# Performance work log

Measured on AMD Instinct MI355X. Metric: run time of the kernel, lower is better.

The kernel has to match this reference:

```python
import jax, jax.numpy as jnp
import numpy as np

DIM = 2048
DT_RANK = 64
DIM_INNER = 2048
D_STATE = 32
B_SZ = 4
L = 2048


def setup_inputs() -> dict:
    key = jax.random.key(0)
    ks = jax.random.split(key, 6)
    x = jax.random.normal(ks[0], (B_SZ, L, DIM), dtype=jnp.float32)
    z = jax.random.normal(ks[1], (B_SZ, L, DIM_INNER), dtype=jnp.float32)
    # proj_bc: Linear(dim, dt_rank + 2*d_state, bias=False)
    W_bc = jax.random.normal(ks[2], (DT_RANK + 2 * D_STATE, DIM), dtype=jnp.float32) * (DIM ** -0.5)
    # dt_proj: maps dt_rank -> dim_inner (as intended in Mamba)
    W_dt = jax.random.normal(ks[3], (DIM_INNER, DT_RANK), dtype=jnp.float32) * (DT_RANK ** -0.5)
    b_dt = jax.random.normal(ks[4], (DIM_INNER,), dtype=jnp.float32) * 0.1
    # A = arange(1, d_state+1) repeated per channel; A_log = log(A)
    A_log = jnp.log(jnp.tile(jnp.arange(1, D_STATE + 1, dtype=jnp.float32), (DIM_INNER, 1)))
    D_param = jnp.ones((DIM_INNER,), dtype=jnp.float32)
    return {"x": x, "z": z, "W_bc": W_bc, "W_dt": W_dt, "b_dt": b_dt, "A_log": A_log, "D_param": D_param}


def _selective_scan(u, delta, A, Bm, Cm, D_param):
    # u, delta: [b, l, d]; Bm, Cm: [b, l, n]; A: [d, n]; D_param: [d]
    def step(h, inp):
        delta_t, B_t, C_t, u_t = inp  # [b,d], [b,n], [b,n], [b,d]
        dA = jnp.exp(delta_t[:, :, None] * A[None])          # [b, d, n]
        dBu = (delta_t * u_t)[:, :, None] * B_t[:, None, :]  # [b, d, n]
        h = dA * h + dBu
        y_t = jnp.einsum('bdn,bn->bd', h, C_t)
        return h, y_t

    b = u.shape[0]
    h0 = jnp.zeros((b, A.shape[0], A.shape[1]), dtype=u.dtype)
    xs = (jnp.moveaxis(delta, 1, 0), jnp.moveaxis(Bm, 1, 0),
          jnp.moveaxis(Cm, 1, 0), jnp.moveaxis(u, 1, 0))
    _, ys = jax.lax.scan(step, h0, xs)          # ys: [l, b, d]
    y = jnp.moveaxis(ys, 0, 1)                  # [b, l, d]
    return y + u * D_param[None, None, :]


def reference(x, z, W_bc, W_dt, b_dt, A_log, D_param):
    A = -jnp.exp(A_log)                                      # [d, n]
    deltaBC = jnp.einsum('bld,od->blo', x, W_bc)             # [b, l, r+2n]
    dt_r = deltaBC[..., :DT_RANK]
    Bm = deltaBC[..., DT_RANK:DT_RANK + D_STATE]             # [b, l, n]
    Cm = deltaBC[..., DT_RANK + D_STATE:]                    # [b, l, n]
    dt = jnp.einsum('blr,dr->bld', dt_r, W_dt)               # [b, l, d]
    delta = jax.nn.softplus(dt + b_dt[None, None, :])        # delta_softplus + delta_bias
    y = _selective_scan(x, delta, A, Bm, Cm, D_param)        # [b, l, d]
    return y
```

## Files before the change

### kernel.cpp

```cpp
#include <hip/hip_runtime.h>

#define L_SEQ 2048
#define NDIM 2048
#define DINNER 2048
#define NSTATE 32
#define BSZ 4
#define DTR 64
#define NROWS (BSZ * L_SEQ)
#define TCH 32

typedef short bf16x8 __attribute__((ext_vector_type(8)));
typedef float f32x4 __attribute__((ext_vector_type(4)));
typedef float f32x2 __attribute__((ext_vector_type(2)));
typedef unsigned int uint_t;

#if __has_builtin(__builtin_amdgcn_exp2f)
#define EXP2(v) __builtin_amdgcn_exp2f(v)
#else
#define EXP2(v) exp2f(v)
#endif
#define LOG2E 1.44269504f

__device__ __forceinline__ uint_t bf1(float a) {
  uint_t u = __float_as_uint(a);
  return (u + 0x7FFFu + ((u >> 16) & 1u)) >> 16;
}
__device__ __forceinline__ uint_t pkbf(float a, float b) {
  return bf1(a) | (bf1(b) << 16);
}

#define WBC_ELEMS (128 * NDIM)
#define WDT_ELEMS (DINNER * DTR)
__global__ __launch_bounds__(256) void k_conv(const float* __restrict__ Wbc,
                                              const float* __restrict__ Wdt,
                                              unsigned short* __restrict__ o) {
  const int i = blockIdx.x * 256 + threadIdx.x;
  if (i < WBC_ELEMS)
    o[i] = (unsigned short)bf1(Wbc[i]);
  else
    o[i] = (unsigned short)bf1(Wdt[i - WBC_ELEMS]);
}

__global__ __launch_bounds__(512) void k_dbc_mfma(const float* __restrict__ x,
                                                  const unsigned short* __restrict__ Wb,
                                                  float* __restrict__ dbc) {
  __shared__ unsigned short xl[32][72];
  __shared__ unsigned short wl[128][72];
  const int tid = threadIdx.x;
  const int wave = tid >> 6, lane = tid & 63;
  const int row0 = blockIdx.x * 32;
  const int wrow0 = (wave & 1) * 16;
  const int wcol0 = (wave >> 1) * 32;
  const int fr = lane & 15, fk = (lane >> 4) * 8;

  f32x4 acc[2];
#pragma unroll
  for (int i = 0; i < 2; ++i) acc[i] = (f32x4)(0.f);

  const int xr = tid >> 4, xk = (tid & 15) * 4;
  const int wc = tid & 127, wh = (tid >> 7) * 16;

  for (int kb = 0; kb < NDIM; kb += 64) {
    const float4 xa = *(const float4*)(x + (size_t)(row0 + xr) * NDIM + kb + xk);
    uint4 wv0 = *(const uint4*)(Wb + (size_t)wc * NDIM + kb + wh);
    uint4 wv1 = *(const uint4*)(Wb + (size_t)wc * NDIM + kb + wh + 8);
    __syncthreads();
    uint2 xp = {pkbf(xa.x, xa.y), pkbf(xa.z, xa.w)};
    *(uint2*)&xl[xr][xk] = xp;
    *(uint4*)&wl[wc][wh] = wv0;
    *(uint4*)&wl[wc][wh + 8] = wv1;
    __syncthreads();
#pragma unroll
    for (int ks = 0; ks < 2; ++ks) {
      const bf16x8 af = *(const bf16x8*)&xl[wrow0 + fr][ks * 32 + fk];
#pragma unroll
      for (int nt = 0; nt < 2; ++nt) {
        const bf16x8 bfv = *(const bf16x8*)&wl[wcol0 + nt * 16 + fr][ks * 32 + fk];
        acc[nt] = __builtin_amdgcn_mfma_f32_16x16x32_bf16(af, bfv, acc[nt], 0, 0, 0);
      }
    }
  }
#pragma unroll
  for (int nt = 0; nt < 2; ++nt)
#pragma unroll
    for (int reg = 0; reg < 4; ++reg)
      dbc[(size_t)(row0 + wrow0 + (lane >> 4) * 4 + reg) * 128 + wcol0 + nt * 16 + fr] =
          acc[nt][reg];
}

__global__ __launch_bounds__(256) void k_dt_mfma(const float* __restrict__ dbc,
                                                 const unsigned short* __restrict__ Wd,
                                                 const float* __restrict__ bdt,
                                                 float* __restrict__ dy) {
  __shared__ unsigned short al[32][72];
  const int tid = threadIdx.x;
  const int wave = tid >> 6, lane = tid & 63;
  const int row0 = blockIdx.y * 32;
  const int c0 = blockIdx.x * 256;
  const int wrow0 = (wave & 1) * 16;
  const int wc0 = c0 + (wave >> 1) * 128;
  const int fr = lane & 15, fk = (lane >> 4) * 8;

  {
    const int ar = tid >> 3, ak = (tid & 7) * 8;
    const float4 pa = *(const float4*)(dbc + (size_t)(row0 + ar) * 128 + ak);
    const float4 pb = *(const float4*)(dbc + (size_t)(row0 + ar) * 128 + ak + 4);
    uint4 ap = {pkbf(pa.x, pa.y), pkbf(pa.z, pa.w), pkbf(pb.x, pb.y), pkbf(pb.z, pb.w)};
    *(uint4*)&al[ar][ak] = ap;
  }
  __syncthreads();

  f32x4 acc[8];
#pragma unroll
  for (int i = 0; i < 8; ++i) acc[i] = (f32x4)(0.f);

#pragma unroll
  for (int ks = 0; ks < 2; ++ks) {
    const bf16x8 af = *(const bf16x8*)&al[wrow0 + fr][ks * 32 + fk];
#pragma unroll
    for (int nt = 0; nt < 8; ++nt) {
      const int col = wc0 + nt * 16 + fr;
      const bf16x8 bfv = *(const bf16x8*)(Wd + (size_t)col * 64 + ks * 32 + fk);
      acc[nt] = __builtin_amdgcn_mfma_f32_16x16x32_bf16(af, bfv, acc[nt], 0, 0, 0);
    }
  }

#pragma unroll
  for (int nt = 0; nt < 8; ++nt) {
    const int col = wc0 + nt * 16 + fr;
    const float bias = bdt[col];
#pragma unroll
    for (int reg = 0; reg < 4; ++reg) {
      const float v = acc[nt][reg] + bias;
      const float sp = (v > 20.f) ? v : __logf(1.f + __expf(v));
      dy[(size_t)(row0 + wrow0 + (lane >> 4) * 4 + reg) * DINNER + col] = sp;
    }
  }
}

__global__ __launch_bounds__(256) void k_dbc(const float* __restrict__ x,
                                             const float* __restrict__ Wbc,
                                             float* __restrict__ dbc) {
  __shared__ float xs[32][36];
  __shared__ float ws[32][132];
  const int tid = threadIdx.x;
  const int tx = tid & 31;
  const int ty = tid >> 5;
  const int row0 = blockIdx.x * 32;
  float acc[4][4];
#pragma unroll
  for (int i = 0; i < 4; ++i)
#pragma unroll
    for (int j = 0; j < 4; ++j) acc[i][j] = 0.f;
  for (int kb = 0; kb < NDIM; kb += 32) {
    {
      const int r = tid >> 3;
      const int k0 = (tid & 7) * 4;
      const float4 v = *(const float4*)(x + (size_t)(row0 + r) * NDIM + kb + k0);
      *(float4*)&xs[r][k0] = v;
    }
    {
      const int col = tid & 127;
      const int k0 = (tid >> 7) * 16;
#pragma unroll
      for (int j = 0; j < 4; ++j) {
        const float4 v = *(const float4*)(Wbc + (size_t)col * NDIM + kb + k0 + j * 4);
        ws[k0 + j * 4 + 0][col] = v.x;
        ws[k0 + j * 4 + 1][col] = v.y;
        ws[k0 + j * 4 + 2][col] = v.z;
        ws[k0 + j * 4 + 3][col] = v.w;
      }
    }
    __syncthreads();
#pragma unroll
    for (int k = 0; k < 32; k += 4) {
      float a_[4][4];
#pragma unroll
      for (int i = 0; i < 4; ++i) {
        const float4 av = *(const float4*)&xs[ty * 4 + i][k];
        a_[i][0] = av.x; a_[i][1] = av.y; a_[i][2] = av.z; a_[i][3] = av.w;
      }
#pragma unroll
      for (int kk = 0; kk < 4; ++kk) {
        const float4 bv = *(const float4*)&ws[k + kk][tx * 4];
        float b_[4] = {bv.x, bv.y, bv.z, bv.w};
#pragma unroll
        for (int i = 0; i < 4; ++i)
#pragma unroll
          for (int j = 0; j < 4; ++j)
            acc[i][j] = fmaf(a_[i][kk], b_[j], acc[i][j]);
      }
    }
    __syncthreads();
  }
#pragma unroll
  for (int i = 0; i < 4; ++i) {
    float4 o = {acc[i][0], acc[i][1], acc[i][2], acc[i][3]};
    *(float4*)(dbc + (size_t)(row0 + ty * 4 + i) * 128 + tx * 4) = o;
  }
}

__global__ __launch_bounds__(256) void k_dt(const float* __restrict__ dbc,
                                            const float* __restrict__ Wdt,
                                            const float* __restrict__ bdt,
                                            float* dy) {
  __shared__ float asn[16][68];
  __shared__ float wst[64][132];
  const int tid = threadIdx.x;
  const int tx = tid & 31;
  const int ty = tid >> 5;
  const int row0 = blockIdx.y * 16;
  const int col0 = blockIdx.x * 128;
  {
    const int r = tid >> 4;
    const int k0 = (tid & 15) * 4;
    const float4 v = *(const float4*)(dbc + (size_t)(row0 + r) * 128 + k0);
    *(float4*)&asn[r][k0] = v;
  }
  {
    const int col = tid & 127;
    const int k0 = (tid >> 7) * 32;
#pragma unroll
    for (int j = 0; j < 8; ++j) {
      const float4 v = *(const float4*)(Wdt + (size_t)(col0 + col) * 64 + k0 + j * 4);
      wst[k0 + j * 4 + 0][col] = v.x;
      wst[k0 + j * 4 + 1][col] = v.y;
      wst[k0 + j * 4 + 2][col] = v.z;
      wst[k0 + j * 4 + 3][col] = v.w;
    }
  }
  __syncthreads();
  float acc[2][4];
#pragma unroll
  for (int i = 0; i < 2; ++i)
#pragma unroll
    for (int j = 0; j < 4; ++j) acc[i][j] = 0.f;
#pragma unroll
  for (int k = 0; k < 64; k += 4) {
    float a_[2][4];
#pragma unroll
    for (int i = 0; i < 2; ++i) {
      const float4 av = *(const float4*)&asn[ty * 2 + i][k];
      a_[i][0] = av.x; a_[i][1] = av.y; a_[i][2] = av.z; a_[i][3] = av.w;
    }
#pragma unroll
    for (int kk = 0; kk < 4; ++kk) {
      const float4 bv = *(const float4*)&wst[k + kk][tx * 4];
      float b_[4] = {bv.x, bv.y, bv.z, bv.w};
#pragma unroll
      for (int i = 0; i < 2; ++i)
#pragma unroll
        for (int j = 0; j < 4; ++j)
          acc[i][j] = fmaf(a_[i][kk], b_[j], acc[i][j]);
    }
  }
  const int c = col0 + tx * 4;
  const float4 bb = *(const float4*)(bdt + c);
  const float bias[4] = {bb.x, bb.y, bb.z, bb.w};
#pragma unroll
  for (int i = 0; i < 2; ++i) {
    float o[4];
#pragma unroll
    for (int j = 0; j < 4; ++j) {
      const float v = acc[i][j] + bias[j];
      o[j] = (v > 20.f) ? v : __logf(1.f + __expf(v));
    }
    float4 ov = {o[0], o[1], o[2], o[3]};
    *(float4*)(dy + (size_t)(row0 + ty * 2 + i) * DINNER + c) = ov;
  }
}

template <int CTRL>
__device__ __forceinline__ float dpp_mov(float v) {
  return __int_as_float(
      __builtin_amdgcn_update_dpp(0, __float_as_int(v), CTRL, 0xF, 0xF, true));
}
__device__ __forceinline__ float red16(float p) {
  p += dpp_mov<0xB1>(p);
  p += dpp_mov<0x4E>(p);
  p += dpp_mov<0x141>(p);
  p += dpp_mov<0x140>(p);
  return p;
}

__global__ __launch_bounds__(256) void k_scanp(const float* __restrict__ x,
                                               const float* __restrict__ dbc,
                                               const float* __restrict__ Alog,
                                               const float* __restrict__ Dpar,
                                               float* __restrict__ dy) {
  __shared__ float sDU[2][16][68];
  __shared__ float sBCp[2][32][68];
  __shared__ float sY[2][32][17];

  const int tid = threadIdx.x;
  const int ln = tid & 15, ch = tid >> 4;
  const int dd = tid & 15, tl = tid >> 4;
  const int nb = tid & 31, tq = tid >> 5;
  const int dg = blockIdx.x & 127;
  const int b = blockIdx.x >> 7;
  const int d0 = dg * 16;
  const int NCHK = L_SEQ / TCH;

  f32x2 An2;
  An2.x = -__expf(Alog[(size_t)(d0 + ch) * NSTATE + ln]) * LOG2E;
  An2.y = -__expf(Alog[(size_t)(d0 + ch) * NSTATE + ln + 16]) * LOG2E;
  const float Dd = Dpar[d0 + dd];
  const size_t segbase = (size_t)b * L_SEQ;

  const int bccol = (nb & 15) * 4 + (nb >> 4) * 2;

  float u0, u1;
  {
    const size_t rX0 = (segbase + tl) * DINNER + d0 + dd;
    const size_t rX1 = (segbase + tl + 16) * DINNER + d0 + dd;
    const float dv0 = dy[rX0], uv0 = x[rX0];
    const float dv1 = dy[rX1], uv1 = x[rX1];
    *(float2*)&sDU[0][dd][(tl >> 1) * 4 + (tl & 1) * 2] = make_float2(dv0, dv0 * uv0);
    *(float2*)&sDU[0][(tl >> 1) + 8][0] = *(float2*)&sDU[0][(tl >> 1) + 8][0];
    *(float2*)&sDU[0][dd][((tl + 16) >> 1) * 4 + (tl & 1) * 2] =
        make_float2(dv1, dv1 * uv1);
    u0 = uv0;
    u1 = uv1;
#pragma unroll
    for (int k = 0; k < 4; ++k) {
      const int t = tq + k * 8;
      const size_t rB = (segbase + t) * 128 + 64 + nb;
      *(float2*)&sBCp[0][t][bccol] = make_float2(dbc[rB], dbc[rB + 32]);
    }
  }
  __syncthreads();

  f32x2 h = (f32x2)(0.f);
  for (int c = 0; c < NCHK; ++c) {
    const int cb = c & 1;
    float dn0 = 0.f, un0 = 0.f, dn1 = 0.f, un1 = 0.f;
    float2 bcx[4];
#pragma unroll
    for (int k = 0; k < 4; ++k) bcx[k] = make_float2(0.f, 0.f);
    if (c < NCHK - 1) {
      const size_t rX0 = (segbase + (c + 1) * TCH + tl) * DINNER + d0 + dd;
      const size_t rX1 = (segbase + (c + 1) * TCH + tl + 16) * DINNER + d0 + dd;
      dn0 = dy[rX0];
      un0 = x[rX0];
      dn1 = dy[rX1];
      un1 = x[rX1];
#pragma unroll
      for (int k = 0; k < 4; ++k) {
        const size_t rB = (segbase + (c + 1) * TCH + tq + k * 8) * 128 + 64 + nb;
        bcx[k] = make_float2(dbc[rB], dbc[rB + 32]);
      }
    }

    const float* pDU = &sDU[cb][ch][0];
    const float* pBC = &sBCp[cb][0][ln * 4];
    float yv0 = 0.f, yv1 = 0.f;
#pragma unroll
    for (int t2 = 0; t2 < TCH / 2; ++t2) {
      const float4 du = *(const float4*)(pDU + t2 * 4);
      const float4 b0 = *(const float4*)(pBC + (2 * t2) * 68);
      const float4 b1 = *(const float4*)(pBC + (2 * t2 + 1) * 68);
      {
        const int t = 2 * t2;
        f32x2 ea = An2 * du.x;
        f32x2 dA;
        dA.x = EXP2(ea.x);
        dA.y = EXP2(ea.y);
        f32x2 Bp;
        Bp.x = b0.x;
        Bp.y = b0.z;
        f32x2 Cp;
        Cp.x = b0.y;
        Cp.y = b0.w;
        h = dA * h + Bp * du.y;
        const f32x2 pp = h * Cp;
        const float p = red16(pp.x + pp.y);
        if (t < 16)
          yv0 = (ln == t) ? p : yv0;
        else
          yv1 = (ln == t - 16) ? p : yv1;
      }
      {
        const int t = 2 * t2 + 1;
        f32x2 ea = An2 * du.z;
        f32x2 dA;
        dA.x = EXP2(ea.x);
        dA.y = EXP2(ea.y);
        f32x2 Bp;
        Bp.x = b1.x;
        Bp.y = b1.z;
        f32x2 Cp;
        Cp.x = b1.y;
        Cp.y = b1.w;
        h = dA * h + Bp * du.w;
        const f32x2 pp = h * Cp;
        const float p = red16(pp.x + pp.y);
        if (t < 16)
          yv0 = (ln == t) ? p : yv0;
        else
          yv1 = (ln == t - 16) ? p : yv1;
      }
    }
    sY[cb][ln][ch] = yv0;
    sY[cb][ln + 16][ch] = yv1;

    if (c < NCHK - 1) {
      *(float2*)&sDU[cb ^ 1][dd][(tl >> 1) * 4 + (tl & 1) * 2] =
          make_float2(dn0, dn0 * un0);
      *(float2*)&sDU[cb ^ 1][dd][((tl + 16) >> 1) * 4 + (tl & 1) * 2] =
          make_float2(dn1, dn1 * un1);
#pragma unroll
      for (int k = 0; k < 4; ++k)
        *(float2*)&sBCp[cb ^ 1][tq + k * 8][bccol] = bcx[k];
    }
    __syncthreads();

    dy[(segbase + c * TCH + tl) * DINNER + d0 + dd] = fmaf(u0, Dd, sY[cb][tl][dd]);
    dy[(segbase + c * TCH + tl + 16) * DINNER + d0 + dd] =
        fmaf(u1, Dd, sY[cb][tl + 16][dd]);
    u0 = un0;
    u1 = un1;
  }
}

extern "C" void kernel_launch(void* const* d_in, const int* in_sizes, int n_in,
                              void* d_out, int out_size, void* d_ws, size_t ws_size,
                              hipStream_t stream) {
  const float* x    = (const float*)d_in[0];
  const float* Wbc  = (const float*)d_in[2];
  const float* Wdt  = (const float*)d_in[3];
  const float* bdt  = (const float*)d_in[4];
  const float* Alog = (const float*)d_in[5];
  const float* Dpar = (const float*)d_in[6];
  float* dy  = (float*)d_out;
  float* dbc = (float*)d_ws;

  const size_t DBC_BYTES = (size_t)NROWS * 128 * 4;
  const size_t WCONV_BYTES = (size_t)(WBC_ELEMS + WDT_ELEMS) * 2;

  const bool mfma_ok = ws_size >= DBC_BYTES + WCONV_BYTES;

  if (mfma_ok) {
    unsigned short* Wb = (unsigned short*)((char*)d_ws + DBC_BYTES);
    unsigned short* Wd = Wb + WBC_ELEMS;
    hipLaunchKernelGGL(k_conv, dim3((WBC_ELEMS + WDT_ELEMS) / 256), dim3(256), 0,
                       stream, Wbc, Wdt, Wb);
    hipLaunchKernelGGL(k_dbc_mfma, dim3(NROWS / 32), dim3(512), 0, stream,
                       x, Wb, dbc);
    hipLaunchKernelGGL(k_dt_mfma, dim3(DINNER / 256, NROWS / 32), dim3(256), 0,
                       stream, dbc, Wd, bdt, dy);
  } else {
    hipLaunchKernelGGL(k_dbc, dim3(NROWS / 32), dim3(256), 0, stream, x, Wbc, dbc);
    hipLaunchKernelGGL(k_dt, dim3(DINNER / 128, NROWS / 16), dim3(256), 0, stream,
                       dbc, Wdt, bdt, dy);
  }

  hipLaunchKernelGGL(k_scanp, dim3(BSZ * DINNER / 16), dim3(256), 0, stream,
                     x, dbc, Alog, Dpar, dy);
}
```

Measured before the change: 253.6 us.

## Split selective scan into two sequence halves with carried state pass

Splits the scan over the sequence into two halves. A first kernel scans the first half per channel group with no outputs and stores the final hidden state to a workspace buffer. A second kernel then runs both halves in parallel, doubling the block count, with the second half seeded from the stored state. This exposes more parallelism on a latency-bound recurrence, at the cost of recomputing the first-half recurrence and launching an extra kernel.

New measurement: 272.1 us. 1.07x slower.

```diff
diff --git a/kernel.cpp b/kernel.cpp
--- a/kernel.cpp
+++ b/kernel.cpp
@@ -8,6 +8,7 @@
 #define DTR 64
 #define NROWS (BSZ * L_SEQ)
 #define TCH 32
+#define LHALF (L_SEQ / 2)
 
 typedef short bf16x8 __attribute__((ext_vector_type(8)));
 typedef float f32x4 __attribute__((ext_vector_type(4)));
@@ -283,14 +284,13 @@
   return p;
 }
 
-__global__ __launch_bounds__(256) void k_scanp(const float* __restrict__ x,
-                                               const float* __restrict__ dbc,
-                                               const float* __restrict__ Alog,
-                                               const float* __restrict__ Dpar,
-                                               float* __restrict__ dy) {
+__global__ __launch_bounds__(256) void k_p1p(const float* __restrict__ x,
+                                             const float* __restrict__ dlt,
+                                             const float* __restrict__ dbc,
+                                             const float* __restrict__ Alog,
+                                             float* __restrict__ hbuf) {
   __shared__ float sDU[2][16][68];
-  __shared__ float sBCp[2][32][68];
-  __shared__ float sY[2][32][17];
+  __shared__ float sBp[2][32][34];
 
   const int tid = threadIdx.x;
   const int ln = tid & 15, ch = tid >> 4;
@@ -299,14 +299,116 @@
   const int dg = blockIdx.x & 127;
   const int b = blockIdx.x >> 7;
   const int d0 = dg * 16;
-  const int NCHK = L_SEQ / TCH;
+  const int NCHK = LHALF / TCH;
+
+  f32x2 An2;
+  An2.x = -__expf(Alog[(size_t)(d0 + ch) * NSTATE + ln]) * LOG2E;
+  An2.y = -__expf(Alog[(size_t)(d0 + ch) * NSTATE + ln + 16]) * LOG2E;
+  const size_t segbase = (size_t)b * L_SEQ;
+  const int bcol = (nb & 15) * 2 + (nb >> 4);
+
+  {
+    const size_t rX0 = (segbase + tl) * DINNER + d0 + dd;
+    const size_t rX1 = (segbase + tl + 16) * DINNER + d0 + dd;
+    const float dv0 = dlt[rX0], uv0 = x[rX0];
+    const float dv1 = dlt[rX1], uv1 = x[rX1];
+    *(float2*)&sDU[0][dd][(tl >> 1) * 4 + (tl & 1) * 2] = make_float2(dv0, dv0 * uv0);
+    *(float2*)&sDU[0][dd][((tl + 16) >> 1) * 4 + (tl & 1) * 2] =
+        make_float2(dv1, dv1 * uv1);
+#pragma unroll
+    for (int k = 0; k < 4; ++k) {
+      const int t = tq + k * 8;
+      sBp[0][t][bcol] = dbc[(segbase + t) * 128 + 64 + nb];
+    }
+  }
+  __syncthreads();
+
+  f32x2 h = (f32x2)(0.f);
+  for (int c = 0; c < NCHK; ++c) {
+    const int cb = c & 1;
+    float dn0 = 0.f, un0 = 0.f, dn1 = 0.f, un1 = 0.f;
+    float bnx[4] = {0.f, 0.f, 0.f, 0.f};
+    if (c < NCHK - 1) {
+      const size_t rX0 = (segbase + (c + 1) * TCH + tl) * DINNER + d0 + dd;
+      const size_t rX1 = (segbase + (c + 1) * TCH + tl + 16) * DINNER + d0 + dd;
+      dn0 = dlt[rX0];
+      un0 = x[rX0];
+      dn1 = dlt[rX1];
+      un1 = x[rX1];
+#pragma unroll
+      for (int k = 0; k < 4; ++k)
+        bnx[k] = dbc[(segbase + (c + 1) * TCH + tq + k * 8) * 128 + 64 + nb];
+    }
+
+    const float* pDU = &sDU[cb][ch][0];
+    const float* pBp = &sBp[cb][0][ln * 2];
+#pragma unroll
+    for (int t2 = 0; t2 < TCH / 2; ++t2) {
+      const float4 du = *(const float4*)(pDU + t2 * 4);
+      const float2 b0 = *(const float2*)(pBp + (2 * t2) * 34);
+      const float2 b1 = *(const float2*)(pBp + (2 * t2 + 1) * 34);
+      {
+        f32x2 ea = An2 * du.x;
+        f32x2 dA;
+        dA.x = EXP2(ea.x);
+        dA.y = EXP2(ea.y);
+        f32x2 Bp;
+        Bp.x = b0.x;
+        Bp.y = b0.y;
+        h = dA * h + Bp * du.y;
+      }
+      {
+        f32x2 ea = An2 * du.z;
+        f32x2 dA;
+        dA.x = EXP2(ea.x);
+        dA.y = EXP2(ea.y);
+        f32x2 Bp;
+        Bp.x = b1.x;
+        Bp.y = b1.y;
+        h = dA * h + Bp * du.w;
+      }
+    }
+
+    if (c < NCHK - 1) {
+      *(float2*)&sDU[cb ^ 1][dd][(tl >> 1) * 4 + (tl & 1) * 2] =
+          make_float2(dn0, dn0 * un0);
+      *(float2*)&sDU[cb ^ 1][dd][((tl + 16) >> 1) * 4 + (tl & 1) * 2] =
+          make_float2(dn1, dn1 * un1);
+#pragma unroll
+      for (int k = 0; k < 4; ++k) sBp[cb ^ 1][tq + k * 8][bcol] = bnx[k];
+    }
+    __syncthreads();
+  }
+
+  const size_t hb = ((size_t)b * DINNER + d0 + ch) * NSTATE;
+  hbuf[hb + ln] = h.x;
+  hbuf[hb + ln + 16] = h.y;
+}
+
+template <int SEG>
+__device__ __forceinline__ void scanp_body(const float* __restrict__ x,
+                                           const float* __restrict__ dbc,
+                                           const float* __restrict__ Alog,
+                                           const float* __restrict__ Dpar,
+                                           const float* __restrict__ hbuf,
+                                           float* __restrict__ dy, int bid,
+                                           float (*sDU)[16][68],
+                                           float (*sBCp)[32][68],
+                                           float (*sY)[32][17]) {
+  const int tid = threadIdx.x;
+  const int ln = tid & 15, ch = tid >> 4;
+  const int dd = tid & 15, tl = tid >> 4;
+  const int nb = tid & 31, tq = tid >> 5;
+  const int dg = bid & 127;
+  const int b = bid >> 7;
+  const int d0 = dg * 16;
+  const int NCHK = LHALF / TCH;
 
   f32x2 An2;
   An2.x = -__expf(Alog[(size_t)(d0 + ch) * NSTATE + ln]) * LOG2E;
   An2.y = -__expf(Alog[(size_t)(d0 + ch) * NSTATE + ln + 16]) * LOG2E;
   const float Dd = Dpar[d0 + dd];
-  const size_t segbase = (size_t)b * L_SEQ;
-
+  const size_t segbase = (size_t)b * L_SEQ + SEG * LHALF;
   const int bccol = (nb & 15) * 4 + (nb >> 4) * 2;
 
   float u0, u1;
@@ -316,7 +418,6 @@
     const float dv0 = dy[rX0], uv0 = x[rX0];
     const float dv1 = dy[rX1], uv1 = x[rX1];
     *(float2*)&sDU[0][dd][(tl >> 1) * 4 + (tl & 1) * 2] = make_float2(dv0, dv0 * uv0);
-    *(float2*)&sDU[0][(tl >> 1) + 8][0] = *(float2*)&sDU[0][(tl >> 1) + 8][0];
     *(float2*)&sDU[0][dd][((tl + 16) >> 1) * 4 + (tl & 1) * 2] =
         make_float2(dv1, dv1 * uv1);
     u0 = uv0;
@@ -328,9 +429,15 @@
       *(float2*)&sBCp[0][t][bccol] = make_float2(dbc[rB], dbc[rB + 32]);
     }
   }
+
+  f32x2 h = (f32x2)(0.f);
+  if (SEG == 1) {
+    const size_t hb = ((size_t)b * DINNER + d0 + ch) * NSTATE;
+    h.x = hbuf[hb + ln];
+    h.y = hbuf[hb + ln + 16];
+  }
   __syncthreads();
 
-  f32x2 h = (f32x2)(0.f);
   for (int c = 0; c < NCHK; ++c) {
     const int cb = c & 1;
     float dn0 = 0.f, un0 = 0.f, dn1 = 0.f, un1 = 0.f;
@@ -422,6 +529,160 @@
   }
 }
 
+__global__ __launch_bounds__(256) void k_p2p(const float* __restrict__ x,
+                                             const float* __restrict__ dbc,
+                                             const float* __restrict__ Alog,
+                                             const float* __restrict__ Dpar,
+                                             const float* __restrict__ hbuf,
+                                             float* __restrict__ dy) {
+  __shared__ float sDU[2][16][68];
+  __shared__ float sBCp[2][32][68];
+  __shared__ float sY[2][32][17];
+  const int bx = blockIdx.x;
+  if (bx < BSZ * DINNER / 16)
+    scanp_body<0>(x, dbc, Alog, Dpar, hbuf, dy, bx, sDU, sBCp, sY);
+  else
+    scanp_body<1>(x, dbc, Alog, Dpar, hbuf, dy, bx - BSZ * DINNER / 16, sDU,
+                  sBCp, sY);
+}
+
+__global__ __launch_bounds__(256) void k_scanp(const float* __restrict__ x,
+                                               const float* __restrict__ dbc,
+                                               const float* __restrict__ Alog,
+                                               const float* __restrict__ Dpar,
+                                               float* __restrict__ dy) {
+  __shared__ float sDU[2][16][68];
+  __shared__ float sBCp[2][32][68];
+  __shared__ float sY[2][32][17];
+
+  const int tid = threadIdx.x;
+  const int ln = tid & 15, ch = tid >> 4;
+  const int dd = tid & 15, tl = tid >> 4;
+  const int nb = tid & 31, tq = tid >> 5;
+  const int dg = blockIdx.x & 127;
+  const int b = blockIdx.x >> 7;
+  const int d0 = dg * 16;
+  const int NCHK = L_SEQ / TCH;
+
+  f32x2 An2;
+  An2.x = -__expf(Alog[(size_t)(d0 + ch) * NSTATE + ln]) * LOG2E;
+  An2.y = -__expf(Alog[(size_t)(d0 + ch) * NSTATE + ln + 16]) * LOG2E;
+  const float Dd = Dpar[d0 + dd];
+  const size_t segbase = (size_t)b * L_SEQ;
+  const int bccol = (nb & 15) * 4 + (nb >> 4) * 2;
+
+  float u0, u1;
+  {
+    const size_t rX0 = (segbase + tl) * DINNER + d0 + dd;
+    const size_t rX1 = (segbase + tl + 16) * DINNER + d0 + dd;
+    const float dv0 = dy[rX0], uv0 = x[rX0];
+    const float dv1 = dy[rX1], uv1 = x[rX1];
+    *(float2*)&sDU[0][dd][(tl >> 1) * 4 + (tl & 1) * 2] = make_float2(dv0, dv0 * uv0);
+    *(float2*)&sDU[0][dd][((tl + 16) >> 1) * 4 + (tl & 1) * 2] =
+        make_float2(dv1, dv1 * uv1);
+    u0 = uv0;
+    u1 = uv1;
+#pragma unroll
+    for (int k = 0; k < 4; ++k) {
+      const int t = tq + k * 8;
+      const size_t rB = (segbase + t) * 128 + 64 + nb;
+      *(float2*)&sBCp[0][t][bccol] = make_float2(dbc[rB], dbc[rB + 32]);
+    }
+  }
+  __syncthreads();
+
+  f32x2 h = (f32x2)(0.f);
+  for (int c = 0; c < NCHK; ++c) {
+    const int cb = c & 1;
+    float dn0 = 0.f, un0 = 0.f, dn1 = 0.f, un1 = 0.f;
+    float2 bcx[4];
+#pragma unroll
+    for (int k = 0; k < 4; ++k) bcx[k] = make_float2(0.f, 0.f);
+    if (c < NCHK - 1) {
+      const size_t rX0 = (segbase + (c + 1) * TCH + tl) * DINNER + d0 + dd;
+      const size_t rX1 = (segbase + (c + 1) * TCH + tl + 16) * DINNER + d0 + dd;
+      dn0 = dy[rX0];
+      un0 = x[rX0];
+      dn1 = dy[rX1];
+      un1 = x[rX1];
+#pragma unroll
+      for (int k = 0; k < 4; ++k) {
+        const size_t rB = (segbase + (c + 1) * TCH + tq + k * 8) * 128 + 64 + nb;
+        bcx[k] = make_float2(dbc[rB], dbc[rB + 32]);
+      }
+    }
+
+    const float* pDU = &sDU[cb][ch][0];
+    const float* pBC = &sBCp[cb][0][ln * 4];
+    float yv0 = 0.f, yv1 = 0.f;
+#pragma unroll
+    for (int t2 = 0; t2 < TCH / 2; ++t2) {
+      const float4 du = *(const float4*)(pDU + t2 * 4);
+      const float4 b0 = *(const float4*)(pBC + (2 * t2) * 68);
+      const float4 b1 = *(const float4*)(pBC + (2 * t2 + 1) * 68);
+      {
+        const int t = 2 * t2;
+        f32x2 ea = An2 * du.x;
+        f32x2 dA;
+        dA.x = EXP2(ea.x);
+        dA.y = EXP2(ea.y);
+        f32x2 Bp;
+        Bp.x = b0.x;
+        Bp.y = b0.z;
+        f32x2 Cp;
+        Cp.x = b0.y;
+        Cp.y = b0.w;
+        h = dA * h + Bp * du.y;
+        const f32x2 pp = h * Cp;
+        const float p = red16(pp.x + pp.y);
+        if (t < 16)
+          yv0 = (ln == t) ? p : yv0;
+        else
+          yv1 = (ln == t - 16) ? p : yv1;
+      }
+      {
+        const int t = 2 * t2 + 1;
+        f32x2 ea = An2 * du.z;
+        f32x2 dA;
+        dA.x = EXP2(ea.x);
+        dA.y = EXP2(ea.y);
+        f32x2 Bp;
+        Bp.x = b1.x;
+        Bp.y = b1.z;
+        f32x2 Cp;
+        Cp.x = b1.y;
+        Cp.y = b1.w;
+        h = dA * h + Bp * du.w;
+        const f32x2 pp = h * Cp;
+        const float p = red16(pp.x + pp.y);
+        if (t < 16)
+          yv0 = (ln == t) ? p : yv0;
+        else
+          yv1 = (ln == t - 16) ? p : yv1;
+      }
+    }
+    sY[cb][ln][ch] = yv0;
+    sY[cb][ln + 16][ch] = yv1;
+
+    if (c < NCHK - 1) {
+      *(float2*)&sDU[cb ^ 1][dd][(tl >> 1) * 4 + (tl & 1) * 2] =
+          make_float2(dn0, dn0 * un0);
+      *(float2*)&sDU[cb ^ 1][dd][((tl + 16) >> 1) * 4 + (tl & 1) * 2] =
+          make_float2(dn1, dn1 * un1);
+#pragma unroll
+      for (int k = 0; k < 4; ++k)
+        *(float2*)&sBCp[cb ^ 1][tq + k * 8][bccol] = bcx[k];
+    }
+    __syncthreads();
+
+    dy[(segbase + c * TCH + tl) * DINNER + d0 + dd] = fmaf(u0, Dd, sY[cb][tl][dd]);
+    dy[(segbase + c * TCH + tl + 16) * DINNER + d0 + dd] =
+        fmaf(u1, Dd, sY[cb][tl + 16][dd]);
+    u0 = un0;
+    u1 = un1;
+  }
+}
+
 extern "C" void kernel_launch(void* const* d_in, const int* in_sizes, int n_in,
                               void* d_out, int out_size, void* d_ws, size_t ws_size,
                               hipStream_t stream) {
@@ -436,8 +697,11 @@
 
   const size_t DBC_BYTES = (size_t)NROWS * 128 * 4;
   const size_t WCONV_BYTES = (size_t)(WBC_ELEMS + WDT_ELEMS) * 2;
+  const size_t H_OFF = 8u << 20;
+  const size_t H_BYTES = (size_t)BSZ * DINNER * NSTATE * 4;
 
   const bool mfma_ok = ws_size >= DBC_BYTES + WCONV_BYTES;
+  const bool seg_ok = ws_size >= H_OFF + H_BYTES;
 
   if (mfma_ok) {
     unsigned short* Wb = (unsigned short*)((char*)d_ws + DBC_BYTES);
@@ -454,6 +718,14 @@
                        dbc, Wdt, bdt, dy);
   }
 
-  hipLaunchKernelGGL(k_scanp, dim3(BSZ * DINNER / 16), dim3(256), 0, stream,
-                     x, dbc, Alog, Dpar, dy);
-}
+  if (seg_ok) {
+    float* hbuf = (float*)((char*)d_ws + H_OFF);
+    hipLaunchKernelGGL(k_p1p, dim3(BSZ * DINNER / 16), dim3(256), 0, stream,
+                       x, dy, dbc, Alog, hbuf);
+    hipLaunchKernelGGL(k_p2p, dim3(2 * BSZ * DINNER / 16), dim3(256), 0, stream,
+                       x, dbc, Alog, Dpar, hbuf, dy);
+  } else {
+    hipLaunchKernelGGL(k_scanp, dim3(BSZ * DINNER / 16), dim3(256), 0, stream,
+                       x, dbc, Alog, Dpar, dy);
+  }
+}
```
